# Kernel tuning notes

Hardware: AMD Instinct MI355X
Metric: run time of the kernel (lower is better)

The kernel has to match this reference:

```python
import jax, jax.numpy as jnp
import numpy as np

B, S, D = 2, 2048, 2048
H, Dh = 16, 128  # qkv_features = H*Dh = 2048
NEG = -1e10


def setup_inputs() -> dict:
    key = jax.random.key(0)
    k1, k2, k3 = jax.random.split(key, 3)
    x = jax.random.normal(k1, (B, S, D), dtype=jnp.float32)
    # variance_scaling(1.0, 'fan_in', 'normal') ~ std = 1/sqrt(fan_in)
    Wqkv = jax.random.normal(k2, (D, 3 * H * Dh), dtype=jnp.float32) / np.sqrt(D)
    bqkv = jnp.zeros((3 * H * Dh,), dtype=jnp.float32)
    Wout = jax.random.normal(k3, (H * Dh, D), dtype=jnp.float32) / np.sqrt(H * Dh)
    bout = jnp.zeros((D,), dtype=jnp.float32)
    return {"x": x, "Wqkv": Wqkv, "bqkv": bqkv, "Wout": Wout, "bout": bout}


def reference(x, Wqkv, bqkv, Wout, bout):
    b, s, _ = x.shape
    # fused QKV projection
    qkv = x @ Wqkv + bqkv                                   # [B, S, 3*H*Dh]
    qkv = qkv.reshape(b, s, 3, H, Dh).transpose(2, 0, 3, 1, 4)  # [3, B, H, S, Dh]
    q, k, v = qkv[0], qkv[1], qkv[2]
    scale = 1.0 / jnp.sqrt(jnp.asarray(Dh, dtype=x.dtype))
    # Each query chunk attends to the full key sequence with a causal mask,
    # which is mathematically full causal attention.
    scores = jnp.einsum('bhqd,bhkd->bhqk', q, k) * scale    # [B, H, S, S]
    causal = jnp.arange(s)[None, :] <= jnp.arange(s)[:, None]  # k <= q
    scores = jnp.where(causal[None, None, :, :], scores, NEG)
    weights = jax.nn.softmax(scores, axis=-1)
    out = jnp.einsum('bhqk,bhkd->bhqd', weights, v)         # [B, H, S, Dh]
    out = out.transpose(0, 2, 1, 3).reshape(b, s, H * Dh)
    return out @ Wout + bout
```

## Files before the change

kernel.cpp:

```cpp
#include <hip/hip_runtime.h>


typedef unsigned short u16;
typedef __attribute__((ext_vector_type(8))) short bf16x8;
typedef __attribute__((ext_vector_type(4))) float f32x4;

#define MFMA(a, b, c) __builtin_amdgcn_mfma_f32_16x16x32_bf16((a), (b), (c), 0, 0, 0)

__device__ __forceinline__ u16 f2bf(float f) {
    unsigned u = __builtin_bit_cast(unsigned, f);
    u += 0x7fffu + ((u >> 16) & 1u);
    return (u16)(u >> 16);
}

__device__ __forceinline__ void gload16(const void* g, void* l) {
    __builtin_amdgcn_global_load_lds(
        (const __attribute__((address_space(1))) void*)g,
        (__attribute__((address_space(3))) void*)l, 16, 0, 0);
}


__global__ __launch_bounds__(256) void k_cast(const float* __restrict__ src,
                                              u16* __restrict__ dst, int n4) {
    int i = blockIdx.x * 256 + threadIdx.x;
    if (i >= n4) return;
    float4 a = ((const float4*)src)[i];
    ushort4 r;
    r.x = f2bf(a.x); r.y = f2bf(a.y); r.z = f2bf(a.z); r.w = f2bf(a.w);
    ((ushort4*)dst)[i] = r;
}

__global__ __launch_bounds__(256) void k_castT(const float* __restrict__ src,
                                               u16* __restrict__ dst, int rows, int cols) {
    __shared__ float t[32][33];
    int c0 = blockIdx.x * 32, r0 = blockIdx.y * 32;
    int tx = threadIdx.x, ty = threadIdx.y;
#pragma unroll
    for (int i = 0; i < 4; ++i)
        t[ty + 8 * i][tx] = src[(size_t)(r0 + ty + 8 * i) * cols + (c0 + tx)];
    __syncthreads();
#pragma unroll
    for (int i = 0; i < 4; ++i)
        dst[(size_t)(c0 + ty + 8 * i) * rows + (r0 + tx)] = f2bf(t[tx][ty + 8 * i]);
}

__global__ __launch_bounds__(256) void k_transv(const u16* __restrict__ v,
                                                u16* __restrict__ vT) {
    __shared__ u16 t[32][33];
    int head = blockIdx.z;
    int s0 = blockIdx.x * 32, d0 = blockIdx.y * 32;
    const u16* vp = v + (size_t)head * 2048 * 128;
    u16* op = vT + (size_t)head * 128 * 2048;
    int tx = threadIdx.x, ty = threadIdx.y;
#pragma unroll
    for (int i = 0; i < 4; ++i)
        t[ty + 8 * i][tx] = vp[(size_t)(s0 + ty + 8 * i) * 128 + d0 + tx];
    __syncthreads();
#pragma unroll
    for (int i = 0; i < 4; ++i)
        op[(size_t)(d0 + 8 * i + ty) * 2048 + (s0 + tx)] = t[tx][ty + 8 * i];
}


template <int K>
__device__ __forceinline__ void gemm_core64(const u16* __restrict__ A,
                                            const u16* __restrict__ BT,
                                            int m0, int n0,
                                            f32x4 (&acc)[4][4],
                                            u16* As, u16* Bs) {
    const int tid = threadIdx.x, wave = tid >> 6, lane = tid & 63;
    const int wr = (wave >> 1) * 64, wc = (wave & 1) * 64;
    char* AsB = (char*)As;
    char* BsB = (char*)Bs;
    for (int k0 = 0; k0 < K; k0 += 64) {
        __syncthreads();
#pragma unroll
        for (int i = 0; i < 4; ++i) {
            int cb = (i * 4 + wave) * 64;
            int d = (cb + lane) * 16;
            int row = d >> 7;
            int co = (d & 127) ^ ((row & 7) << 4);
            gload16(A + (size_t)(m0 + row) * K + k0 + (co >> 1), AsB + cb * 16);
            gload16(BT + (size_t)(n0 + row) * K + k0 + (co >> 1), BsB + cb * 16);
        }
        __syncthreads();
        bf16x8 a[2][4], b[2][4];
#pragma unroll
        for (int ks = 0; ks < 2; ++ks)
#pragma unroll
            for (int m = 0; m < 4; ++m) {
                int row = wr + m * 16 + (lane & 15);
                a[ks][m] = *(const bf16x8*)(AsB +
                    ((row * 128 + ks * 64 + (lane >> 4) * 16) ^ ((row & 7) << 4)));
            }
#pragma unroll
        for (int ks = 0; ks < 2; ++ks)
#pragma unroll
            for (int n = 0; n < 4; ++n) {
                int row = wc + n * 16 + (lane & 15);
                b[ks][n] = *(const bf16x8*)(BsB +
                    ((row * 128 + ks * 64 + (lane >> 4) * 16) ^ ((row & 7) << 4)));
            }
        __builtin_amdgcn_s_setprio(1);
#pragma unroll
        for (int ks = 0; ks < 2; ++ks)
#pragma unroll
            for (int m = 0; m < 4; ++m)
#pragma unroll
                for (int n = 0; n < 4; ++n)
                    acc[m][n] = MFMA(a[ks][m], b[ks][n], acc[m][n]);
        __builtin_amdgcn_s_setprio(0);
    }
}

__global__ __launch_bounds__(256) void k_gemm_qkv(const u16* __restrict__ A,
                                                  const u16* __restrict__ BT,
                                                  const float* __restrict__ bias,
                                                  u16* __restrict__ q,
                                                  u16* __restrict__ kbuf,
                                                  u16* __restrict__ v) {
    __shared__ __align__(16) u16 As[128 * 64];
    __shared__ __align__(16) u16 Bs[128 * 64];
    f32x4 acc[4][4] = {};
    const int orig = blockIdx.y * 48 + blockIdx.x;
    const int xcd = orig & 7, idx = orig >> 3;
    const int n_blk = xcd * 6 + idx % 6, m_blk = idx / 6;
    const int m0 = m_blk * 128, n0 = n_blk * 128;
    gemm_core64<2048>(A, BT, m0, n0, acc, As, Bs);

    const int tid = threadIdx.x, wave = tid >> 6, lane = tid & 63;
    const int wr = (wave >> 1) * 64, wc = (wave & 1) * 64;
    const int t = n0 >> 11;
    u16* dst = (t == 0) ? q : (t == 1) ? kbuf : v;
#pragma unroll
    for (int m = 0; m < 4; ++m)
#pragma unroll
        for (int n = 0; n < 4; ++n)
#pragma unroll
            for (int j = 0; j < 4; ++j) {
                int gr = m0 + wr + m * 16 + (lane >> 4) * 4 + j;
                int gc = n0 + wc + n * 16 + (lane & 15);
                float val = acc[m][n][j] + bias[gc];
                int bb = gr >> 11, s = gr & 2047;
                int rem = gc & 2047, h = rem >> 7, d = rem & 127;
                dst[((size_t)(bb * 16 + h) * 2048 + s) * 128 + d] = f2bf(val);
            }
}

__global__ __launch_bounds__(256) void k_gemm_out(const u16* __restrict__ A,
                                                  const u16* __restrict__ BT,
                                                  const float* __restrict__ bias,
                                                  float* __restrict__ out) {
    __shared__ __align__(16) u16 As[128 * 64];
    __shared__ __align__(16) u16 Bs[128 * 64];
    f32x4 acc[4][4] = {};
    const int orig = blockIdx.y * 16 + blockIdx.x;
    const int nb = (orig & 7) * 64 + (orig >> 3);
    const int m0 = (nb / 16) * 128, n0 = (nb % 16) * 128;
    gemm_core64<2048>(A, BT, m0, n0, acc, As, Bs);

    const int tid = threadIdx.x, wave = tid >> 6, lane = tid & 63;
    const int wr = (wave >> 1) * 64, wc = (wave & 1) * 64;
#pragma unroll
    for (int m = 0; m < 4; ++m)
#pragma unroll
        for (int n = 0; n < 4; ++n)
#pragma unroll
            for (int j = 0; j < 4; ++j) {
                int gr = m0 + wr + m * 16 + (lane >> 4) * 4 + j;
                int gc = n0 + wc + n * 16 + (lane & 15);
                out[(size_t)gr * 2048 + gc] = acc[m][n][j] + bias[gc];
            }
}

__global__ __launch_bounds__(256) void k_attn(const u16* __restrict__ q,
                                              const u16* __restrict__ k,
                                              const u16* __restrict__ vT,
                                              u16* __restrict__ o) {
    __shared__ __align__(16) u16 KsA[2 * 64 * 128];
    __shared__ __align__(16) u16 VsA[2 * 128 * 64];
    __shared__ __align__(16) u16 PsA[4 * 16 * 64];
    char* ksB = (char*)KsA;
    char* vsB = (char*)VsA;

    const int tid = threadIdx.x, wave = tid >> 6, lane = tid & 63;
    char* psB = (char*)PsA + wave * 2048;

    const int lin = blockIdx.x;
    const int dd = (lin & 7) * 64 + (lin >> 3);
    const int head = dd >> 4, pair = dd & 15;

    const u16* qh = q + (size_t)head * 2048 * 128;
    const u16* kh = k + (size_t)head * 2048 * 128;
    const u16* vh = vT + (size_t)head * 128 * 2048;
    const int bb = head >> 4, hh = head & 15;
    const float qscale = 0.1275293562566334f;
    const float MFIX = 20.f;

    bf16x8 ones;
#pragma unroll
    for (int e = 0; e < 8; ++e) ones[e] = (short)0x3F80;

    auto stage = [&](int kv0, int bufsel) {
        char* kd = ksB + bufsel * 16384;
        char* vd = vsB + bufsel * 16384;
#pragma unroll
        for (int i = 0; i < 4; ++i) {
            int cb = (i * 4 + wave) * 64;
            int d = (cb + lane) * 16;
            int r = d >> 8;
            int co = (d & 255) ^ ((r & 7) << 4);
            gload16(kh + (size_t)(kv0 + r) * 128 + (co >> 1), kd + cb * 16);
        }
#pragma unroll
        for (int i = 0; i < 4; ++i) {
            int cb = (i * 4 + wave) * 64;
            int d = (cb + lane) * 16;
            int vr = d >> 7;
            int co = (d & 127) ^ ((vr & 7) << 4);
            gload16(vh + (size_t)vr * 2048 + kv0 + (co >> 1), vd + cb * 16);
        }
    };

#pragma unroll 1
    for (int qsel = 0; qsel < 2; ++qsel) {
        const int qi = qsel ? (31 - pair) : pair;
        const int q0 = qi * 64;
        const int ntile = qi + 1;

        bf16x8 qf[4];
        const int qr = q0 + wave * 16 + (lane & 15);
#pragma unroll
        for (int kt = 0; kt < 4; ++kt)
            qf[kt] = *(const bf16x8*)(qh + (size_t)qr * 128 + kt * 32 + (lane >> 4) * 8);

        f32x4 o_acc[8] = {};
        f32x4 l_r = {};

        stage(0, 0);
        int buf = 0;

#pragma unroll 1
        for (int t = 0; t < ntile; ++t) {
            const int kv0 = t * 64;
            if (t + 1 < ntile) {
                stage(kv0 + 64, buf ^ 1);
                asm volatile("s_waitcnt vmcnt(8)" ::: "memory");
            } else {
                asm volatile("s_waitcnt vmcnt(0)" ::: "memory");
            }
            __builtin_amdgcn_s_barrier();
            char* kb_ = ksB + buf * 16384;
            char* vb_ = vsB + buf * 16384;

            f32x4 s_acc[4] = {};
            __builtin_amdgcn_s_setprio(1);
#pragma unroll
            for (int c = 0; c < 4; ++c) {
                int row = c * 16 + (lane & 15);
#pragma unroll
                for (int kt = 0; kt < 4; ++kt) {
                    bf16x8 kbf = *(const bf16x8*)(kb_ +
                        ((row * 256 + kt * 64 + (lane >> 4) * 16) ^ ((row & 7) << 4)));
                    s_acc[c] = MFMA(qf[kt], kbf, s_acc[c]);
                }
            }
            __builtin_amdgcn_s_setprio(0);

            const bool maskblk = (kv0 + 64 > q0);
#pragma unroll
            for (int j = 0; j < 4; ++j) {
                int qg = q0 + wave * 16 + (lane >> 4) * 4 + j;
#pragma unroll
                for (int c = 0; c < 4; ++c) {
                    float sv = fmaf(s_acc[c][j], qscale, -MFIX);
                    if (maskblk && (kv0 + c * 16 + (lane & 15)) > qg) sv = -1e30f;
                    s_acc[c][j] = exp2f(sv);
                }
            }

#pragma unroll
            for (int c = 0; c < 4; ++c)
#pragma unroll
                for (int j = 0; j < 4; ++j) {
                    int row = (lane >> 4) * 4 + j;
                    *(u16*)(psB + ((row * 128 + (c * 16 + (lane & 15)) * 2) ^ ((row & 7) << 4)))
                        = f2bf(s_acc[c][j]);
                }
            bf16x8 pf[2];
#pragma unroll
            for (int kt = 0; kt < 2; ++kt) {
                int row2 = lane & 15;
                pf[kt] = *(const bf16x8*)(psB +
                    ((row2 * 128 + kt * 64 + (lane >> 4) * 16) ^ ((row2 & 7) << 4)));
            }

            __builtin_amdgcn_s_setprio(1);
            l_r = MFMA(pf[0], ones, l_r);
            l_r = MFMA(pf[1], ones, l_r);
#pragma unroll
            for (int c2 = 0; c2 < 8; ++c2) {
#pragma unroll
                for (int kt = 0; kt < 2; ++kt) {
                    int row = c2 * 16 + (lane & 15);
                    bf16x8 vf = *(const bf16x8*)(vb_ +
                        ((row * 128 + kt * 64 + (lane >> 4) * 16) ^ ((row & 7) << 4)));
                    o_acc[c2] = MFMA(pf[kt], vf, o_acc[c2]);
                }
            }
            __builtin_amdgcn_s_setprio(0);

            __builtin_amdgcn_s_barrier();
            buf ^= 1;
        }

        float linv[4];
#pragma unroll
        for (int j = 0; j < 4; ++j) linv[j] = 1.0f / l_r[j];
#pragma unroll
        for (int c2 = 0; c2 < 8; ++c2)
#pragma unroll
            for (int j = 0; j < 4; ++j) {
                int qg = q0 + wave * 16 + (lane >> 4) * 4 + j;
                int d2 = c2 * 16 + (lane & 15);
                o[((size_t)(bb * 2048 + qg)) * 2048 + hh * 128 + d2]
                    = f2bf(o_acc[c2][j] * linv[j]);
            }
    }
}


extern "C" void kernel_launch(void* const* d_in, const int* in_sizes, int n_in,
                              void* d_out, int out_size, void* d_ws, size_t ws_size,
                              hipStream_t stream) {
    const float* x    = (const float*)d_in[0];
    const float* Wqkv = (const float*)d_in[1];
    const float* bqkv = (const float*)d_in[2];
    const float* Wout = (const float*)d_in[3];
    const float* bout = (const float*)d_in[4];
    float* out = (float*)d_out;

    char* ws = (char*)d_ws;
    const size_t SZ = 16777216;
    u16* q   = (u16*)(ws);
    u16* kb  = (u16*)(ws + SZ);
    u16* v   = (u16*)(ws + 2 * SZ);
    u16* vT  = (u16*)(ws + 3 * SZ);
    u16* ao  = v;
    u16* xb  = (u16*)(ws + 4 * SZ);
    u16* WqT = (u16*)(ws + 5 * SZ);
    u16* WoT = (u16*)(ws + 5 * SZ + 25165824);

    k_cast<<<dim3(8192), dim3(256), 0, stream>>>(x, xb, 2097152);
    k_castT<<<dim3(192, 64), dim3(32, 8), 0, stream>>>(Wqkv, WqT, 2048, 6144);
    k_castT<<<dim3(64, 64), dim3(32, 8), 0, stream>>>(Wout, WoT, 2048, 2048);
    k_gemm_qkv<<<dim3(48, 32), dim3(256), 0, stream>>>(xb, WqT, bqkv, q, kb, v);
    k_transv<<<dim3(64, 4, 32), dim3(32, 8), 0, stream>>>(v, vT);
    k_attn<<<dim3(512), dim3(256), 0, stream>>>(q, kb, vT, ao);
    k_gemm_out<<<dim3(16, 32), dim3(256), 0, stream>>>(ao, WoT, bout, out);
}
```

Measured before the change: 249.3 us.

## Double-buffer LDS tiles in output projection GEMM to overlap loads with MFMA

Adds a double-buffered variant of the 128x128x64 GEMM core that issues the next K-tile's global-to-LDS loads before computing on the current tile, using one barrier per iteration. Only the output projection kernel switches to it, with LDS doubled to 64 KB per block. The goal is to hide global load latency behind MFMA work; the larger LDS footprint may lower occupancy.

```diff
diff --git a/kernel.cpp b/kernel.cpp
--- a/kernel.cpp
+++ b/kernel.cpp
@@ -110,6 +110,78 @@
                 for (int n = 0; n < 4; ++n)
                     acc[m][n] = MFMA(a[ks][m], b[ks][n], acc[m][n]);
         __builtin_amdgcn_s_setprio(0);
+    }
+}
+
+
+template <int K>
+__device__ __forceinline__ void gemm_core64_db(const u16* __restrict__ A,
+                                               const u16* __restrict__ BT,
+                                               int m0, int n0,
+                                               f32x4 (&acc)[4][4],
+                                               char* AsB, char* BsB) {
+    const int tid = threadIdx.x, wave = tid >> 6, lane = tid & 63;
+    const int wr = (wave >> 1) * 64, wc = (wave & 1) * 64;
+
+    auto stage = [&](int k0, int bufsel) {
+        char* ad = AsB + bufsel * 16384;
+        char* bd = BsB + bufsel * 16384;
+#pragma unroll
+        for (int i = 0; i < 4; ++i) {
+            int cb = (i * 4 + wave) * 64;
+            int d = (cb + lane) * 16;
+            int row = d >> 7;
+            int co = (d & 127) ^ ((row & 7) << 4);
+            gload16(A + (size_t)(m0 + row) * K + k0 + (co >> 1), ad + cb * 16);
+            gload16(BT + (size_t)(n0 + row) * K + k0 + (co >> 1), bd + cb * 16);
+        }
+    };
+
+    stage(0, 0);
+    asm volatile("s_waitcnt vmcnt(0)" ::: "memory");
+    __builtin_amdgcn_s_barrier();
+
+    const int NT = K / 64;
+    int buf = 0;
+#pragma unroll 1
+    for (int t = 0; t < NT; ++t) {
+        const bool pre = (t + 1 < NT);
+        if (pre) stage((t + 1) * 64, buf ^ 1);
+
+        char* ab = AsB + buf * 16384;
+        char* bb = BsB + buf * 16384;
+        bf16x8 a[2][4], b[2][4];
+#pragma unroll
+        for (int ks = 0; ks < 2; ++ks)
+#pragma unroll
+            for (int m = 0; m < 4; ++m) {
+                int row = wr + m * 16 + (lane & 15);
+                a[ks][m] = *(const bf16x8*)(ab +
+                    ((row * 128 + ks * 64 + (lane >> 4) * 16) ^ ((row & 7) << 4)));
+            }
+#pragma unroll
+        for (int ks = 0; ks < 2; ++ks)
+#pragma unroll
+            for (int n = 0; n < 4; ++n) {
+                int row = wc + n * 16 + (lane & 15);
+                b[ks][n] = *(const bf16x8*)(bb +
+                    ((row * 128 + ks * 64 + (lane >> 4) * 16) ^ ((row & 7) << 4)));
+            }
+        __builtin_amdgcn_s_setprio(1);
+#pragma unroll
+        for (int ks = 0; ks < 2; ++ks)
+#pragma unroll
+            for (int m = 0; m < 4; ++m)
+#pragma unroll
+                for (int n = 0; n < 4; ++n)
+                    acc[m][n] = MFMA(a[ks][m], b[ks][n], acc[m][n]);
+        __builtin_amdgcn_s_setprio(0);
+
+        if (pre) {
+            asm volatile("s_waitcnt vmcnt(0)" ::: "memory");
+            __builtin_amdgcn_s_barrier();
+        }
+        buf ^= 1;
     }
 }
 
@@ -151,13 +223,13 @@
                                                   const u16* __restrict__ BT,
                                                   const float* __restrict__ bias,
                                                   float* __restrict__ out) {
-    __shared__ __align__(16) u16 As[128 * 64];
-    __shared__ __align__(16) u16 Bs[128 * 64];
+    __shared__ __align__(16) char AsB[2 * 16384];
+    __shared__ __align__(16) char BsB[2 * 16384];
     f32x4 acc[4][4] = {};
     const int orig = blockIdx.y * 16 + blockIdx.x;
     const int nb = (orig & 7) * 64 + (orig >> 3);
     const int m0 = (nb / 16) * 128, n0 = (nb % 16) * 128;
-    gemm_core64<2048>(A, BT, m0, n0, acc, As, Bs);
+    gemm_core64_db<2048>(A, BT, m0, n0, acc, AsB, BsB);
 
     const int tid = threadIdx.x, wave = tid >> 6, lane = tid & 63;
     const int wr = (wave >> 1) * 64, wc = (wave & 1) * 64;
```

After: 249.5 us. About the same (+0.1%).
